# Optimization experiments

Measured on AMD Instinct MI355X. Metric: run time of the kernel, lower is better.

## Reference

```python
import jax, jax.numpy as jnp
import numpy as np
from jax import lax

NUM_HEADS = 8
EPS_BN = 1e-5
EPS_LN = 1e-5


def setup_inputs() -> dict:
    key = jax.random.key(0)
    ks = iter(jax.random.split(key, 32))
    C = 512
    R = C // 16  # channel-gate reduction
    HID = 512    # classifier hidden
    NC = 1       # num_classes

    def gn(shape, scale=0.02):
        return (jax.random.normal(next(ks), shape, dtype=jnp.float32) * scale)

    inp = {
        "x": jax.random.normal(next(ks), (16, C, 28, 28), dtype=jnp.float32),
        # ChannelGate MLP (Linear(C,R) -> ReLU -> Linear(R,C))
        "mlp_w1": gn((R, C)), "mlp_b1": jnp.zeros((R,), jnp.float32),
        "mlp_w2": gn((C, R)), "mlp_b2": jnp.zeros((C,), jnp.float32),
        # SpatialGate 7x7 conv (2->1, no bias) + BatchNorm2d(1) eval-mode stats
        "sp_w": gn((1, 2, 7, 7)),
        "sp_gamma": jnp.ones((1,), jnp.float32), "sp_beta": jnp.zeros((1,), jnp.float32),
        "sp_mean": jnp.zeros((1,), jnp.float32), "sp_var": jnp.ones((1,), jnp.float32),
        # attention projections
        "wq": gn((C, C)), "bq": jnp.zeros((C,), jnp.float32),
        "wk": gn((C, C)), "bk": jnp.zeros((C,), jnp.float32),
        "wv": gn((C, C)), "bv": jnp.zeros((C,), jnp.float32),
        "wo": gn((C, C)), "bo": jnp.zeros((C,), jnp.float32),
        # classifier: LayerNorm(C) -> Linear(C,512) -> ReLU -> Linear(512,NC)
        "ln_g": jnp.ones((C,), jnp.float32), "ln_b": jnp.zeros((C,), jnp.float32),
        "fc1_w": gn((HID, C)), "fc1_b": jnp.zeros((HID,), jnp.float32),
        "fc2_w": gn((NC, HID)), "fc2_b": jnp.zeros((NC,), jnp.float32),
    }
    return inp


def reference(x, mlp_w1, mlp_b1, mlp_w2, mlp_b2, sp_w, sp_gamma, sp_beta,
              sp_mean, sp_var, wq, bq, wk, bk, wv, bv, wo, bo,
              ln_g, ln_b, fc1_w, fc1_b, fc2_w, fc2_b):
    B, C, H, W = x.shape
    N = H * W
    hd = C // NUM_HEADS

    # ---- CBAM: channel gate (avg + max global pools through shared MLP) ----
    def mlp(p):  # p: [B, C]
        return jax.nn.relu(p @ mlp_w1.T + mlp_b1) @ mlp_w2.T + mlp_b2

    avg_p = x.mean(axis=(2, 3))
    max_p = x.max(axis=(2, 3))
    ch_scale = jax.nn.sigmoid(mlp(avg_p) + mlp(max_p))[:, :, None, None]
    x = x * ch_scale

    # ---- CBAM: spatial gate ----
    comp = jnp.concatenate([x.max(axis=1, keepdims=True),
                            x.mean(axis=1, keepdims=True)], axis=1)  # [B,2,H,W]
    s = lax.conv_general_dilated(comp, sp_w, window_strides=(1, 1),
                                 padding=[(3, 3), (3, 3)],
                                 dimension_numbers=("NCHW", "OIHW", "NCHW"))
    s = (s - sp_mean[None, :, None, None]) * lax.rsqrt(sp_var + EPS_BN)[None, :, None, None]
    s = s * sp_gamma[None, :, None, None] + sp_beta[None, :, None, None]
    x = x * jax.nn.sigmoid(s)

    # ---- multi-head self-attention over HW tokens ----
    xf = x.reshape(B, C, N).transpose(0, 2, 1)  # [B, N, C]

    def heads(w, b):
        return (xf @ w.T + b).reshape(B, N, NUM_HEADS, hd).transpose(0, 2, 1, 3)

    Q, K, V = heads(wq, bq), heads(wk, bk), heads(wv, bv)  # [B, h, N, d]
    scores = jnp.einsum("bhnd,bhmd->bhnm", Q, K) / jnp.sqrt(jnp.float32(hd))
    attn = jax.nn.softmax(scores, axis=-1)  # dropout is identity in eval
    attended = jnp.einsum("bhnm,bhmd->bhnd", attn, V)
    attended = attended.transpose(0, 2, 1, 3).reshape(B, N, C)
    attended = attended @ wo.T + bo
    x = x + attended.transpose(0, 2, 1).reshape(B, C, H, W)

    # ---- classifier head ----
    p = x.mean(axis=(2, 3))  # AdaptiveAvgPool2d(1) + Flatten -> [B, C]
    mu = p.mean(axis=-1, keepdims=True)
    var = p.var(axis=-1, keepdims=True)
    ln = (p - mu) * lax.rsqrt(var + EPS_LN) * ln_g + ln_b
    h = jax.nn.relu(ln @ fc1_w.T + fc1_b)
    return h @ fc2_w.T + fc2_b
```

## Files before the change

kernel.cpp:

```cpp
#include <hip/hip_runtime.h>
#include <math.h>

#define BB 16
#define CC 512
#define HW 784
#define RR 32
#define NHD 8
#define HD 64
#define NT 784
#define NTILE 49
#define SROW 20

#define OFS_AVGP   0
#define OFS_MAXP   8192
#define OFS_CHS    16384
#define OFS_CMAX   24576
#define OFS_CMEAN  37120
#define OFS_SP     49664
#define OFS_P1     62208
#define OFS_ABAR   70400
#define OFS_XG     78592
#define XG_SZ      (BB*CC*HW)
#define OFS_XGT    (OFS_XG + XG_SZ)
#define OFS_QBF    (OFS_XGT + XG_SZ/2)
#define OFS_KBF    (OFS_QBF + XG_SZ/2)
#define OFS_V2     (OFS_KBF + XG_SZ/2)
#define OFS_WF     (OFS_V2 + XG_SZ)
#define OFS_W      OFS_XG
#define OFS_PV     (OFS_XG + 131072)
#define OFS_LNV    (OFS_PV + 8192)
#define OFS_H1     (OFS_LNV + 8192)
#define OFS_CMAXP  (OFS_XG + 262144)
#define OFS_CMEANP (OFS_CMAXP + 200704)

typedef __attribute__((ext_vector_type(8))) short bf16x8;
typedef __attribute__((ext_vector_type(4))) float f32x4;

__device__ __forceinline__ unsigned short f2bf(float x) {
  union { float f; unsigned u; } v; v.f = x;
  unsigned r = v.u + 0x7fffu + ((v.u >> 16) & 1u);
  return (unsigned short)(r >> 16);
}
__device__ __forceinline__ float bf2f(unsigned short x) {
  union { unsigned u; float f; } v; v.u = ((unsigned)x) << 16;
  return v.f;
}

__global__ void k_pool(const float* __restrict__ x, float* avg_p, float* max_p) {
  int wid = threadIdx.x >> 6;
  int lane = threadIdx.x & 63;
  int row = blockIdx.x * 4 + wid;
  const float* xr = x + (size_t)row * HW;
  float s = 0.f, m = -INFINITY;
  for (int i = lane; i < HW; i += 64) { float v = xr[i]; s += v; m = fmaxf(m, v); }
  for (int o = 32; o; o >>= 1) { s += __shfl_down(s, o, 64); m = fmaxf(m, __shfl_down(m, o, 64)); }
  if (lane == 0) { avg_p[row] = s * (1.f/HW); max_p[row] = m; }
}

__global__ void k_chmlp(const float* avg_p, const float* max_p,
                        const float* w1, const float* b1,
                        const float* w2, const float* b2, float* chs) {
  __shared__ float pa[CC], pm[CC], part[256], hr[64];
  int b = blockIdx.x, t = threadIdx.x;
  for (int i = t; i < CC; i += 256) { pa[i] = avg_p[b*CC+i]; pm[i] = max_p[b*CC+i]; }
  __syncthreads();
  {
    int rp = t & 63, ch = t >> 6;
    int r = rp & 31;
    const float* src = (rp < 32) ? pa : pm;
    const float* wr = w1 + (size_t)r*CC + ch*128;
    float s = 0.f;
    #pragma unroll 8
    for (int c = 0; c < 128; c++) s += src[ch*128 + c] * wr[c];
    part[t] = s;
  }
  __syncthreads();
  if (t < 64)
    hr[t] = fmaxf(part[t] + part[64+t] + part[128+t] + part[192+t] + b1[t & 31], 0.f);
  __syncthreads();
  for (int c = t; c < CC; c += 256) {
    float a = 2.f*b2[c];
    const float* wr = w2 + c*RR;
    #pragma unroll
    for (int r = 0; r < RR; r++) a += (hr[r]+hr[32+r])*wr[r];
    chs[b*CC+c] = 1.f/(1.f+__expf(-a));
  }
}

__global__ void k_chgatep(const float* __restrict__ x, const float* __restrict__ chs,
                          float* __restrict__ cmaxp, float* __restrict__ cmeanp) {
  __shared__ float cs[32];
  int b = blockIdx.x, cg = blockIdx.y, t = threadIdx.x;
  if (t < 32) cs[t] = chs[b*CC + cg*32 + t];
  __syncthreads();
  const float* xb = x + ((size_t)b*CC + cg*32)*HW;
  for (int pix = t; pix < HW; pix += 256) {
    float mx = -INFINITY, sm = 0.f;
    #pragma unroll
    for (int c = 0; c < 32; c++) {
      float v = xb[(size_t)c*HW + pix] * cs[c];
      mx = fmaxf(mx, v); sm += v;
    }
    cmaxp[(size_t)(cg*BB + b)*HW + pix] = mx;
    cmeanp[(size_t)(cg*BB + b)*HW + pix] = sm;
  }
}

__global__ void k_cred(const float* __restrict__ cmaxp, const float* __restrict__ cmeanp,
                       float* __restrict__ cmax, float* __restrict__ cmean) {
  int idx = blockIdx.x*256 + threadIdx.x;
  if (idx >= BB*HW) return;
  int b = idx / HW, pix = idx % HW;
  float mx = -INFINITY, sm = 0.f;
  #pragma unroll
  for (int cg = 0; cg < 16; cg++) {
    mx = fmaxf(mx, cmaxp[(size_t)(cg*BB + b)*HW + pix]);
    sm += cmeanp[(size_t)(cg*BB + b)*HW + pix];
  }
  cmax[idx] = mx; cmean[idx] = sm * (1.f/CC);
}

__global__ void k_spconv(const float* __restrict__ cmax, const float* __restrict__ cmean,
                         const float* __restrict__ w,
                         const float* g, const float* be, const float* mu, const float* var,
                         float* sp) {
  int b = blockIdx.x;
  int pix = blockIdx.y*256 + threadIdx.x;
  if (pix >= HW) return;
  int h = pix/28, wd = pix%28;
  float acc = 0.f;
  for (int kh = 0; kh < 7; kh++) {
    int ih = h + kh - 3; if (ih < 0 || ih >= 28) continue;
    for (int kw = 0; kw < 7; kw++) {
      int iw = wd + kw - 3; if (iw < 0 || iw >= 28) continue;
      int ip = ih*28+iw;
      acc += cmax[b*HW+ip]*w[kh*7+kw] + cmean[b*HW+ip]*w[49+kh*7+kw];
    }
  }
  float s = (acc - mu[0])*rsqrtf(var[0]+1e-5f)*g[0] + be[0];
  sp[b*HW+pix] = 1.f/(1.f+__expf(-s));
}

__global__ void k_sfuse(const float* __restrict__ x, const float* __restrict__ chs,
                        const float* __restrict__ sp, unsigned short* __restrict__ xgT,
                        float* __restrict__ p1) {
  __shared__ float cs[CC];
  int nt = blockIdx.x, b = blockIdx.y;
  int t = threadIdx.x, ln = t & 63;
  for (int i = t; i < CC; i += 256) cs[i] = chs[b*CC+i];
  __syncthreads();
  int n = nt*16 + (ln & 15);
  float spv = sp[b*HW + n];
  const float* xb = x + (size_t)b*CC*HW;
  #pragma unroll
  for (int i = 0; i < 4; i++) {
    int s = (t >> 6) + 4*i;
    int c = s*32 + (ln >> 4)*8;
    float v[8]; bf16x8 p;
    #pragma unroll
    for (int j = 0; j < 8; j++) {
      v[j] = xb[(size_t)(c+j)*HW + n] * cs[c+j] * spv;
      p[j] = (short)f2bf(v[j]);
    }
    *(bf16x8*)(xgT + ((((size_t)b*NTILE + nt)*16 + s)*64 + ln)*8) = p;
    #pragma unroll
    for (int j = 0; j < 8; j++) {
      float sv = v[j];
      sv += __shfl_xor(sv, 1, 64); sv += __shfl_xor(sv, 2, 64);
      sv += __shfl_xor(sv, 4, 64); sv += __shfl_xor(sv, 8, 64);
      if ((ln & 15) == 0) atomicAdd(&p1[b*CC + c + j], sv * (1.f/HW));
    }
  }
}

__global__ void k_wfrag(const float* __restrict__ wq, const float* __restrict__ wk,
                        const float* __restrict__ wv, unsigned short* __restrict__ Wf) {
  int idx = blockIdx.x*256 + threadIdx.x;
  int ln = idx & 63;
  int s  = (idx >> 6) & 15;
  int ct = (idx >> 10) & 31;
  int mat = idx >> 15;
  const float* W = (mat==0)? wq : (mat==1)? wk : wv;
  const float* src = W + (size_t)(ct*16 + (ln & 15))*CC + s*32 + (ln >> 4)*8;
  float4 f0 = *(const float4*)src;
  float4 f1 = *(const float4*)(src + 4);
  bf16x8 p;
  p[0]=(short)f2bf(f0.x); p[1]=(short)f2bf(f0.y); p[2]=(short)f2bf(f0.z); p[3]=(short)f2bf(f0.w);
  p[4]=(short)f2bf(f1.x); p[5]=(short)f2bf(f1.y); p[6]=(short)f2bf(f1.z); p[7]=(short)f2bf(f1.w);
  *(bf16x8*)(Wf + (size_t)idx*8) = p;
}

__global__ __launch_bounds__(256) void k_qkv_mfma(
    const unsigned short* __restrict__ xgT, const unsigned short* __restrict__ Wf,
    const float* __restrict__ bq, const float* __restrict__ bk, const float* __restrict__ bv,
    unsigned short* __restrict__ Qbf, unsigned short* __restrict__ Kbf,
    unsigned short* __restrict__ Vbf) {
  __shared__ float Cb[64*132];
  int mt = blockIdx.x;
  int yb = blockIdx.y;
  int b  = blockIdx.z;
  int mat = yb >> 2;
  int c0 = (yb & 3) * 128;
  int t = threadIdx.x, w = t >> 6, ln = t & 63;
  const unsigned short* Ab = xgT + (size_t)b*NTILE*8192;
  const unsigned short* Bb = Wf + (size_t)mat*32*8192;
  int ctg0 = (c0 >> 4) + w*2;
  f32x4 acc[4][2];
  #pragma unroll
  for (int m = 0; m < 4; m++)
    #pragma unroll
    for (int c2 = 0; c2 < 2; c2++) acc[m][c2] = (f32x4){0.f,0.f,0.f,0.f};
  int ntc[4];
  #pragma unroll
  for (int m = 0; m < 4; m++) { int nt = 4*mt + m; ntc[m] = (nt > 48) ? 48 : nt; }
  for (int s = 0; s < 16; s++) {
    bf16x8 bf0 = *(const bf16x8*)(Bb + (size_t)(ctg0*16 + s)*512 + ln*8);
    bf16x8 bf1 = *(const bf16x8*)(Bb + (size_t)((ctg0+1)*16 + s)*512 + ln*8);
    bf16x8 af[4];
    #pragma unroll
    for (int m = 0; m < 4; m++)
      af[m] = *(const bf16x8*)(Ab + (size_t)(ntc[m]*16 + s)*512 + ln*8);
    #pragma unroll
    for (int m = 0; m < 4; m++) {
      acc[m][0] = __builtin_amdgcn_mfma_f32_16x16x32_bf16(af[m], bf0, acc[m][0], 0,0,0);
      acc[m][1] = __builtin_amdgcn_mfma_f32_16x16x32_bf16(af[m], bf1, acc[m][1], 0,0,0);
    }
  }
  #pragma unroll
  for (int m = 0; m < 4; m++)
    #pragma unroll
    for (int c2 = 0; c2 < 2; c2++)
      #pragma unroll
      for (int r = 0; r < 4; r++)
        Cb[(m*16 + (ln>>4)*4 + r)*132 + w*32 + c2*16 + (ln&15)] = acc[m][c2][r];
  __syncthreads();
  const float* bias = (mat==0)? bq : (mat==1)? bk : bv;
  #pragma unroll
  for (int i = 0; i < 4; i++) {
    int p = w*4 + i;
    int ntl = p >> 2, sl = p & 3;
    int nt = 4*mt + ntl;
    if (nt > 48) continue;
    int row = ntl*16 + (ln & 15);
    int col = sl*32 + (ln >> 4)*8;
    float v[8];
    #pragma unroll
    for (int j = 0; j < 8; j++) v[j] = Cb[row*132 + col + j] + bias[c0 + col + j];
    int token = nt*16 + (ln & 15);
    int h = (c0 >> 6) + (sl >> 1);
    int bh = b*NHD + h;
    bf16x8 pk;
    #pragma unroll
    for (int j = 0; j < 8; j++) pk[j] = (short)f2bf(v[j]);
    if (mat < 2) {
      unsigned short* Out = (mat == 0) ? Qbf : Kbf;
      *(bf16x8*)(Out + ((size_t)bh*NTILE + nt)*1024 + (size_t)(sl & 1)*512 + ln*8) = pk;
    } else {
      int d = (sl & 1)*32 + (ln >> 4)*8;
      *(bf16x8*)(Vbf + ((size_t)bh*NT + token)*HD + d) = pk;
    }
  }
}

__global__ __launch_bounds__(256, 2) void k_attn5(const unsigned short* __restrict__ Qbf,
    const unsigned short* __restrict__ Kbf, float* __restrict__ wsum) {
  __shared__ float Se[NTILE*16*SROW];
  __shared__ float l_tmp[64];
  __shared__ float rl[16];
  int bh = blockIdx.x & 127, nt = blockIdx.x >> 7;
  int t = threadIdx.x, w = t >> 6, ln = t & 63;
  const unsigned short* Qb = Qbf + ((size_t)bh*NTILE + nt)*1024;
  const unsigned short* Kb = Kbf + (size_t)bh*NTILE*1024;
  bf16x8 q0 = *(const bf16x8*)(Qb + ln*8);
  bf16x8 q1 = *(const bf16x8*)(Qb + 512 + ln*8);
  float lp[4] = {0.f,0.f,0.f,0.f};
  for (int mt = w; mt < NTILE; mt += 4) {
    bf16x8 k0 = *(const bf16x8*)(Kb + (size_t)mt*1024 + ln*8);
    bf16x8 k1 = *(const bf16x8*)(Kb + (size_t)mt*1024 + 512 + ln*8);
    f32x4 a = {0.f,0.f,0.f,0.f};
    a = __builtin_amdgcn_mfma_f32_16x16x32_bf16(q0, k0, a, 0,0,0);
    a = __builtin_amdgcn_mfma_f32_16x16x32_bf16(q1, k1, a, 0,0,0);
    int m = mt*16 + (ln & 15);
    f32x4 ev;
    #pragma unroll
    for (int r = 0; r < 4; r++) {
      ev[r] = __expf(a[r]*0.125f);
      lp[r] += ev[r];
    }
    *(f32x4*)&Se[m*SROW + (ln>>4)*4] = ev;
  }
  #pragma unroll
  for (int r = 0; r < 4; r++) {
    float v = lp[r];
    v += __shfl_xor(v,1,64); v += __shfl_xor(v,2,64);
    v += __shfl_xor(v,4,64); v += __shfl_xor(v,8,64);
    if ((ln & 15) == 0) l_tmp[w*16 + (ln>>4)*4 + r] = v;
  }
  __syncthreads();
  if (t < 16) rl[t] = 1.f / (l_tmp[t] + l_tmp[16+t] + l_tmp[32+t] + l_tmp[48+t]);
  __syncthreads();
  f32x4 rlv[4];
  #pragma unroll
  for (int j = 0; j < 4; j++) rlv[j] = *(const f32x4*)&rl[j*4];
  for (int m = t; m < NT; m += 256) {
    const float* row = &Se[m*SROW];
    float s = 0.f;
    #pragma unroll
    for (int j = 0; j < 4; j++) {
      f32x4 e = *(const f32x4*)&row[j*4];
      s += e[0]*rlv[j][0] + e[1]*rlv[j][1] + e[2]*rlv[j][2] + e[3]*rlv[j][3];
    }
    atomicAdd(&wsum[bh*NT + m], s);
  }
}

__global__ void k_attn_av(const float* __restrict__ w, const unsigned short* __restrict__ Vm,
                          float* __restrict__ abar) {
  __shared__ float red[256];
  int bh = blockIdx.x, t = threadIdx.x;
  int d = t & 63, chunk = t >> 6;
  float acc = 0.f;
  const unsigned short* vb = Vm + (size_t)bh*NT*HD;
  const float* wb = w + bh*NT;
  for (int m = chunk*196; m < (chunk+1)*196; m++)
    acc += wb[m] * bf2f(vb[(size_t)m*HD + d]);
  red[t] = acc;
  __syncthreads();
  if (t < 64)
    abar[bh*HD + t] = (red[t] + red[64+t] + red[128+t] + red[192+t]) * (1.f/NT);
}

__global__ void k_headA(const float* __restrict__ p1, const float* __restrict__ abar,
                        const float* __restrict__ wo, const float* __restrict__ bo,
                        float* __restrict__ pv) {
  int b = blockIdx.x, cg = blockIdx.y;
  int t = threadIdx.x, w = t >> 6, ln = t & 63;
  float a[8];
  #pragma unroll
  for (int k = 0; k < 8; k++) a[k] = abar[b*CC + ln + 64*k];
  int c0 = cg*64 + w*16;
  for (int i = 0; i < 16; i++) {
    int c = c0 + i;
    const float* wr = wo + (size_t)c*CC;
    float s = 0.f;
    #pragma unroll
    for (int k = 0; k < 8; k++) s += a[k] * wr[ln + 64*k];
    for (int o = 32; o; o >>= 1) s += __shfl_down(s, o, 64);
    if (ln == 0) pv[b*CC + c] = s + bo[c] + p1[b*CC + c];
  }
}

__global__ void k_headB(const float* __restrict__ pv, const float* __restrict__ ln_g,
                        const float* __restrict__ ln_b, float* __restrict__ lnv) {
  int b = blockIdx.x, ln = threadIdx.x;
  float v[8], s = 0.f, s2 = 0.f;
  #pragma unroll
  for (int k = 0; k < 8; k++) { v[k] = pv[b*CC + ln + 64*k]; s += v[k]; s2 += v[k]*v[k]; }
  for (int o = 32; o; o >>= 1) { s += __shfl_down(s, o, 64); s2 += __shfl_down(s2, o, 64); }
  s = __shfl(s, 0, 64); s2 = __shfl(s2, 0, 64);
  float mean = s * (1.f/CC);
  float rs = rsqrtf(s2*(1.f/CC) - mean*mean + 1e-5f);
  #pragma unroll
  for (int k = 0; k < 8; k++) {
    int c = ln + 64*k;
    lnv[b*CC + c] = (v[k]-mean)*rs*ln_g[c] + ln_b[c];
  }
}

__global__ void k_headC(const float* __restrict__ lnv, const float* __restrict__ fc1_w,
                        const float* __restrict__ fc1_b, float* __restrict__ h1) {
  int b = blockIdx.x, cg = blockIdx.y;
  int t = threadIdx.x, w = t >> 6, ln = t & 63;
  float a[8];
  #pragma unroll
  for (int k = 0; k < 8; k++) a[k] = lnv[b*CC + ln + 64*k];
  int c0 = cg*64 + w*16;
  for (int i = 0; i < 16; i++) {
    int c = c0 + i;
    const float* wr = fc1_w + (size_t)c*CC;
    float s = 0.f;
    #pragma unroll
    for (int k = 0; k < 8; k++) s += a[k] * wr[ln + 64*k];
    for (int o = 32; o; o >>= 1) s += __shfl_down(s, o, 64);
    if (ln == 0) h1[b*CC + c] = fmaxf(s + fc1_b[c], 0.f);
  }
}

__global__ void k_headD(const float* __restrict__ h1, const float* __restrict__ fc2_w,
                        const float* __restrict__ fc2_b, float* __restrict__ out) {
  int b = blockIdx.x, ln = threadIdx.x;
  float s = 0.f;
  #pragma unroll
  for (int k = 0; k < 8; k++) s += h1[b*CC + ln + 64*k] * fc2_w[ln + 64*k];
  for (int o = 32; o; o >>= 1) s += __shfl_down(s, o, 64);
  if (ln == 0) out[b] = s + fc2_b[0];
}

extern "C" void kernel_launch(void* const* d_in, const int* in_sizes, int n_in,
                              void* d_out, int out_size, void* d_ws, size_t ws_size,
                              hipStream_t stream) {
  const float* x       = (const float*)d_in[0];
  const float* mlp_w1  = (const float*)d_in[1];
  const float* mlp_b1  = (const float*)d_in[2];
  const float* mlp_w2  = (const float*)d_in[3];
  const float* mlp_b2  = (const float*)d_in[4];
  const float* sp_w    = (const float*)d_in[5];
  const float* sp_g    = (const float*)d_in[6];
  const float* sp_b    = (const float*)d_in[7];
  const float* sp_mu   = (const float*)d_in[8];
  const float* sp_var  = (const float*)d_in[9];
  const float* wq      = (const float*)d_in[10];
  const float* bq      = (const float*)d_in[11];
  const float* wk      = (const float*)d_in[12];
  const float* bk      = (const float*)d_in[13];
  const float* wv      = (const float*)d_in[14];
  const float* bv      = (const float*)d_in[15];
  const float* wo      = (const float*)d_in[16];
  const float* bo      = (const float*)d_in[17];
  const float* ln_g    = (const float*)d_in[18];
  const float* ln_b    = (const float*)d_in[19];
  const float* fc1_w   = (const float*)d_in[20];
  const float* fc1_b   = (const float*)d_in[21];
  const float* fc2_w   = (const float*)d_in[22];
  const float* fc2_b   = (const float*)d_in[23];

  float* ws = (float*)d_ws;
  float* avg_p = ws + OFS_AVGP;
  float* max_p = ws + OFS_MAXP;
  float* chs   = ws + OFS_CHS;
  float* cmax  = ws + OFS_CMAX;
  float* cmean = ws + OFS_CMEAN;
  float* sp    = ws + OFS_SP;
  float* p1    = ws + OFS_P1;
  float* abar  = ws + OFS_ABAR;
  unsigned short* xgT = (unsigned short*)(ws + OFS_XGT);
  unsigned short* Qbf = (unsigned short*)(ws + OFS_QBF);
  unsigned short* Kbf = (unsigned short*)(ws + OFS_KBF);
  unsigned short* Vbf = (unsigned short*)(ws + OFS_V2);
  unsigned short* Wf  = (unsigned short*)(ws + OFS_WF);
  float* wsum  = ws + OFS_W;
  float* pv    = ws + OFS_PV;
  float* lnv   = ws + OFS_LNV;
  float* h1    = ws + OFS_H1;
  float* cmaxp = ws + OFS_CMAXP;
  float* cmeanp= ws + OFS_CMEANP;

  hipMemsetAsync(p1, 0, BB*CC*sizeof(float), stream);
  hipMemsetAsync(wsum, 0, BB*NHD*NT*sizeof(float), stream);

  k_pool   <<<2048, 256, 0, stream>>>(x, avg_p, max_p);
  k_chmlp  <<<BB, 256, 0, stream>>>(avg_p, max_p, mlp_w1, mlp_b1, mlp_w2, mlp_b2, chs);
  k_chgatep<<<dim3(BB,16), 256, 0, stream>>>(x, chs, cmaxp, cmeanp);
  k_cred   <<<49, 256, 0, stream>>>(cmaxp, cmeanp, cmax, cmean);
  k_spconv <<<dim3(BB,4), 256, 0, stream>>>(cmax, cmean, sp_w, sp_g, sp_b, sp_mu, sp_var, sp);
  k_wfrag  <<<384, 256, 0, stream>>>(wq, wk, wv, Wf);
  k_sfuse  <<<dim3(NTILE,BB), 256, 0, stream>>>(x, chs, sp, xgT, p1);
  k_qkv_mfma<<<dim3(13,12,BB), 256, 0, stream>>>(xgT, Wf, bq, bk, bv, Qbf, Kbf, Vbf);
  k_attn5  <<<NTILE*128, 256, 0, stream>>>(Qbf, Kbf, wsum);
  k_attn_av<<<128, 256, 0, stream>>>(wsum, Vbf, abar);
  k_headA  <<<dim3(BB,8), 256, 0, stream>>>(p1, abar, wo, bo, pv);
  k_headB  <<<BB, 64, 0, stream>>>(pv, ln_g, ln_b, lnv);
  k_headC  <<<dim3(BB,8), 256, 0, stream>>>(lnv, fc1_w, fc1_b, h1);
  k_headD  <<<BB, 64, 0, stream>>>(h1, fc2_w, fc2_b, (float*)d_out);
}
```

Measured before the change: 318.9 us.

## Store attention exp scores as fp16 in LDS and process key tiles in pairs

The attention-weight kernel now keeps its exponentiated scores in shared memory as fp16 instead of fp32. This halves LDS use per block, so launch bounds are raised to allow more resident blocks per CU. Each wave now takes a contiguous range of key tiles and handles two per iteration with independent MFMA chains, which gives more instruction-level parallelism. The cost is lower precision in the stored probabilities, and bank-conflict behaviour may change because the row stride is now in half-width units.

```diff
diff --git a/kernel.cpp b/kernel.cpp
--- a/kernel.cpp
+++ b/kernel.cpp
@@ -9,7 +9,7 @@
 #define HD 64
 #define NT 784
 #define NTILE 49
-#define SROW 20
+#define SROWH 20
 
 #define OFS_AVGP   0
 #define OFS_MAXP   8192
@@ -35,6 +35,7 @@
 
 typedef __attribute__((ext_vector_type(8))) short bf16x8;
 typedef __attribute__((ext_vector_type(4))) float f32x4;
+typedef __attribute__((ext_vector_type(4))) _Float16 h16x4;
 
 __device__ __forceinline__ unsigned short f2bf(float x) {
   union { float f; unsigned u; } v; v.f = x;
@@ -262,9 +263,9 @@
   }
 }
 
-__global__ __launch_bounds__(256, 2) void k_attn5(const unsigned short* __restrict__ Qbf,
+__global__ __launch_bounds__(256, 5) void k_attn6(const unsigned short* __restrict__ Qbf,
     const unsigned short* __restrict__ Kbf, float* __restrict__ wsum) {
-  __shared__ float Se[NTILE*16*SROW];
+  __shared__ __align__(16) _Float16 Se[NT*SROWH];
   __shared__ float l_tmp[64];
   __shared__ float rl[16];
   int bh = blockIdx.x & 127, nt = blockIdx.x >> 7;
@@ -274,20 +275,41 @@
   bf16x8 q0 = *(const bf16x8*)(Qb + ln*8);
   bf16x8 q1 = *(const bf16x8*)(Qb + 512 + ln*8);
   float lp[4] = {0.f,0.f,0.f,0.f};
-  for (int mt = w; mt < NTILE; mt += 4) {
-    bf16x8 k0 = *(const bf16x8*)(Kb + (size_t)mt*1024 + ln*8);
-    bf16x8 k1 = *(const bf16x8*)(Kb + (size_t)mt*1024 + 512 + ln*8);
+  int mt0 = w*12, cnt = (w == 3) ? 13 : 12;
+  for (int i = 0; i < cnt; i += 2) {
+    int mtA = mt0 + i;
+    bool hasB = (i + 1) < cnt;
+    int mtB = hasB ? (mtA + 1) : mtA;
+    bf16x8 kA0 = *(const bf16x8*)(Kb + (size_t)mtA*1024 + ln*8);
+    bf16x8 kA1 = *(const bf16x8*)(Kb + (size_t)mtA*1024 + 512 + ln*8);
+    bf16x8 kB0 = *(const bf16x8*)(Kb + (size_t)mtB*1024 + ln*8);
+    bf16x8 kB1 = *(const bf16x8*)(Kb + (size_t)mtB*1024 + 512 + ln*8);
     f32x4 a = {0.f,0.f,0.f,0.f};
-    a = __builtin_amdgcn_mfma_f32_16x16x32_bf16(q0, k0, a, 0,0,0);
-    a = __builtin_amdgcn_mfma_f32_16x16x32_bf16(q1, k1, a, 0,0,0);
-    int m = mt*16 + (ln & 15);
-    f32x4 ev;
+    a = __builtin_amdgcn_mfma_f32_16x16x32_bf16(q0, kA0, a, 0,0,0);
+    a = __builtin_amdgcn_mfma_f32_16x16x32_bf16(q1, kA1, a, 0,0,0);
+    f32x4 c = {0.f,0.f,0.f,0.f};
+    c = __builtin_amdgcn_mfma_f32_16x16x32_bf16(q0, kB0, c, 0,0,0);
+    c = __builtin_amdgcn_mfma_f32_16x16x32_bf16(q1, kB1, c, 0,0,0);
+    int mA = mtA*16 + (ln & 15);
+    h16x4 ea;
     #pragma unroll
     for (int r = 0; r < 4; r++) {
-      ev[r] = __expf(a[r]*0.125f);
-      lp[r] += ev[r];
-    }
-    *(f32x4*)&Se[m*SROW + (ln>>4)*4] = ev;
+      float e = __expf(a[r]*0.125f);
+      lp[r] += e;
+      ea[r] = (_Float16)e;
+    }
+    *(h16x4*)&Se[mA*SROWH + (ln>>4)*4] = ea;
+    if (hasB) {
+      int mB = mtB*16 + (ln & 15);
+      h16x4 eb;
+      #pragma unroll
+      for (int r = 0; r < 4; r++) {
+        float e = __expf(c[r]*0.125f);
+        lp[r] += e;
+        eb[r] = (_Float16)e;
+      }
+      *(h16x4*)&Se[mB*SROWH + (ln>>4)*4] = eb;
+    }
   }
   #pragma unroll
   for (int r = 0; r < 4; r++) {
@@ -303,12 +325,13 @@
   #pragma unroll
   for (int j = 0; j < 4; j++) rlv[j] = *(const f32x4*)&rl[j*4];
   for (int m = t; m < NT; m += 256) {
-    const float* row = &Se[m*SROW];
+    const _Float16* row = &Se[m*SROWH];
     float s = 0.f;
     #pragma unroll
     for (int j = 0; j < 4; j++) {
-      f32x4 e = *(const f32x4*)&row[j*4];
-      s += e[0]*rlv[j][0] + e[1]*rlv[j][1] + e[2]*rlv[j][2] + e[3]*rlv[j][3];
+      h16x4 e = *(const h16x4*)&row[j*4];
+      s += (float)e[0]*rlv[j][0] + (float)e[1]*rlv[j][1]
+         + (float)e[2]*rlv[j][2] + (float)e[3]*rlv[j][3];
     }
     atomicAdd(&wsum[bh*NT + m], s);
   }
@@ -456,7 +479,7 @@
   k_wfrag  <<<384, 256, 0, stream>>>(wq, wk, wv, Wf);
   k_sfuse  <<<dim3(NTILE,BB), 256, 0, stream>>>(x, chs, sp, xgT, p1);
   k_qkv_mfma<<<dim3(13,12,BB), 256, 0, stream>>>(xgT, Wf, bq, bk, bv, Qbf, Kbf, Vbf);
-  k_attn5  <<<NTILE*128, 256, 0, stream>>>(Qbf, Kbf, wsum);
+  k_attn6  <<<NTILE*128, 256, 0, stream>>>(Qbf, Kbf, wsum);
   k_attn_av<<<128, 256, 0, stream>>>(wsum, Vbf, abar);
   k_headA  <<<dim3(BB,8), 256, 0, stream>>>(p1, abar, wo, bo, pv);
   k_headB  <<<BB, 64, 0, stream>>>(pv, ln_g, ln_b, lnv);
```

Result: faster. 301.8 us (-5.4%).
